# Kernel tuning notes

Hardware: AMD Instinct MI355X
Metric: run time of the kernel (lower is better)

Reference implementation:

```python
import jax, jax.numpy as jnp
import numpy as np

B, S, D, H, F = 64, 256, 512, 8, 2048
NB = 2
L = NB + 2 * NB  # blocks_1 (NB) + blocks_2 (2*NB) = 6 attention layers
DH = D // H
FC1, FC2 = 512, 256  # final_fc_dim, final_fc_dim // 2


def setup_inputs() -> dict:
    key = jax.random.key(0)
    ks = jax.random.split(key, 32)
    w = lambda k, shape, s: jax.random.normal(k, shape, dtype=jnp.float32) * s
    sD = D ** -0.5
    return {
        "q_embed_data": w(ks[0], (B, S, D), 1.0),
        "qa_embed_data": w(ks[1], (B, S, D), 1.0),
        "Wq": w(ks[2], (L, D, D), sD), "bq": jnp.zeros((L, D), jnp.float32),
        "Wk": w(ks[3], (L, D, D), sD), "bk": jnp.zeros((L, D), jnp.float32),
        "Wv": w(ks[4], (L, D, D), sD), "bv": jnp.zeros((L, D), jnp.float32),
        "Wo": w(ks[5], (L, D, D), sD), "bo": jnp.zeros((L, D), jnp.float32),
        "gammas": w(ks[6], (L, H), 1.0),
        "ln1_g": jnp.ones((L, D), jnp.float32), "ln1_b": jnp.zeros((L, D), jnp.float32),
        "W1": w(ks[7], (L, D, F), sD), "b1": jnp.zeros((L, F), jnp.float32),
        "W2": w(ks[8], (L, F, D), F ** -0.5), "b2": jnp.zeros((L, D), jnp.float32),
        "ln2_g": jnp.ones((L, D), jnp.float32), "ln2_b": jnp.zeros((L, D), jnp.float32),
        "O1": w(ks[9], (2 * D, FC1), (2 * D) ** -0.5), "bO1": jnp.zeros((FC1,), jnp.float32),
        "O2": w(ks[10], (FC1, FC2), FC1 ** -0.5), "bO2": jnp.zeros((FC2,), jnp.float32),
        "O3": w(ks[11], (FC2, 1), FC2 ** -0.5), "bO3": jnp.zeros((1,), jnp.float32),
    }


def _layer_norm(x, g, b):
    mu = x.mean(-1, keepdims=True)
    var = ((x - mu) ** 2).mean(-1, keepdims=True)
    return (x - mu) * jax.lax.rsqrt(var + 1e-5) * g + b


def _akt_attention(q, k, v, mask, gamma, zero_pad):
    # q,k,v: [B,H,S,DH]; mask: [S,S] bool; gamma: [H]
    neg = jnp.float32(-1e32)
    scores = jnp.einsum('bhqd,bhkd->bhqk', q, k) / np.sqrt(DH).astype(np.float32)
    # monotonic distance-decay (detached in the original): softmax'd scores -> cumulative distance
    sm = jax.nn.softmax(jnp.where(mask, scores, neg), axis=-1) * mask
    sm = jax.lax.stop_gradient(sm)
    distcum = jnp.cumsum(sm, axis=-1)
    disttot = jnp.sum(sm, axis=-1, keepdims=True)
    idx = jnp.arange(S)
    pos = jnp.abs(idx[:, None] - idx[None, :]).astype(jnp.float32)  # |x1 - x2|
    dist = jnp.sqrt(jnp.clip((disttot - distcum) * pos, 0.0, None))
    g = -jax.nn.softplus(gamma)[None, :, None, None]
    total_effect = jnp.clip(jnp.exp(dist * g), 1e-5, 1e5)
    scores = jnp.where(mask, scores * total_effect, neg)
    attn = jax.nn.softmax(scores, axis=-1)
    if zero_pad:
        attn = attn.at[:, :, 0, :].set(0.0)  # zero first query row
    out = jnp.einsum('bhqk,bhkd->bhqd', attn, v)
    return out, attn


def reference(q_embed_data, qa_embed_data, Wq, bq, Wk, bk, Wv, bv, Wo, bo, gammas,
              ln1_g, ln1_b, W1, b1, W2, b2, ln2_g, ln2_b, O1, bO1, O2, bO2, O3, bO3):
    idx = jnp.arange(S)
    mask_incl = idx[:, None] >= idx[None, :]  # mask==1: current + past
    mask_excl = idx[:, None] > idx[None, :]   # mask==0: strictly past

    def block(i, query, key_, vals, incl, zero_pad, apply_pos):
        proj = lambda x, W, b: (x @ W + b).reshape(B, S, H, DH).transpose(0, 2, 1, 3)
        qh, kh, vh = proj(query, Wq[i], bq[i]), proj(key_, Wk[i], bk[i]), proj(vals, Wv[i], bv[i])
        o, attn = _akt_attention(qh, kh, vh, mask_incl if incl else mask_excl, gammas[i], zero_pad)
        o = o.transpose(0, 2, 1, 3).reshape(B, S, D) @ Wo[i] + bo[i]
        q2 = _layer_norm(query + o, ln1_g[i], ln1_b[i])
        if apply_pos:
            h = jax.nn.relu(q2 @ W1[i] + b1[i]) @ W2[i] + b2[i]
            q2 = _layer_norm(q2 + h, ln2_g[i], ln2_b[i])
        return q2, attn

    y = qa_embed_data
    x = q_embed_data
    li = 0
    for _ in range(NB):  # blocks_1: knowledge encoder, self-attn, mask=1
        y, _ = block(li, y, y, y, incl=True, zero_pad=False, apply_pos=True)
        li += 1
    attn = None
    flag_first = True
    for _ in range(2 * NB):  # blocks_2: alternating question self-attn / knowledge retriever
        if flag_first:
            x, _ = block(li, x, x, x, incl=True, zero_pad=False, apply_pos=False)
            flag_first = False
        else:
            x, attn = block(li, x, x, y, incl=False, zero_pad=True, apply_pos=True)
            flag_first = True
        li += 1

    concat_q = jnp.concatenate([x, q_embed_data], axis=-1)  # [B,S,2D]
    h = jax.nn.relu(concat_q @ O1 + bO1)
    h = jax.nn.relu(h @ O2 + bO2)
    preds = jax.nn.sigmoid((h @ O3 + bO3)[..., 0])  # [B,S]
    return preds
```

## Files before the change

### kernel.cpp

```cpp
#include <hip/hip_runtime.h>

typedef unsigned short u16;
typedef unsigned int u32;
typedef short short8 __attribute__((ext_vector_type(8)));
typedef float f32x4 __attribute__((ext_vector_type(4)));

#define DEV static __device__ __forceinline__

DEV u16 f2bf(float f) {
  u32 u = __builtin_bit_cast(u32, f);
  u32 r = u + 0x7FFFu + ((u >> 16) & 1u);
  return (u16)(r >> 16);
}
DEV float bf2f(u16 h) { u32 u = ((u32)h) << 16; return __builtin_bit_cast(float, u); }

DEV u32 cvtpk(float lo, float hi_) {
  u32 r;
  asm("v_cvt_pk_bf16_f32 %0, %1, %2" : "=v"(r) : "v"(lo), "v"(hi_));
  return r;
}

DEV void async16(const u16* g, u16* l) {
  __builtin_amdgcn_global_load_lds((const __attribute__((address_space(1))) void*)g,
                                   (__attribute__((address_space(3))) void*)l, 16, 0, 0);
}

template<bool RELU, bool OUTBF, bool RESID, bool SPLIT3>
__global__ __launch_bounds__(256, 2) void gemm_kernel(
    const u16* __restrict__ A, const u16* __restrict__ A2, int KA,
    int lda, int lda2,
    const u16* __restrict__ Bt, int K,
    const float* __restrict__ bias, const float* __restrict__ resid,
    float* __restrict__ Cf, u16* __restrict__ Cb, u16* __restrict__ Cb2, u16* __restrict__ Cb3,
    int ldc)
{
  __shared__ u16 smem[2][16384];
  const int tid = threadIdx.x, wave = tid >> 6, lane = tid & 63;
  const int m0 = blockIdx.x * 128, n0 = blockIdx.y * 128;
  const int wr = wave >> 1, wc = wave & 1;
  const int lj = lane & 15, hi = lane >> 4;

  f32x4 acc[4][4];
  const f32x4 zz = {0.f, 0.f, 0.f, 0.f};
#pragma unroll
  for (int i = 0; i < 4; i++)
#pragma unroll
    for (int j = 0; j < 4; j++) acc[i][j] = zz;

  const int nkt = K / 64;

  auto stage = [&](int buf, int kt) {
    int kofs = kt * 64;
    const u16* sa; int la;
    if (kofs < KA) { sa = A + kofs; la = lda; }
    else           { sa = A2 + (kofs - KA); la = lda2; }
#pragma unroll
    for (int i = 0; i < 8; i++) {
      int c = wave * 8 + i;
      if (c < 16) {
        const u16* g = sa + (size_t)(m0 + c * 8 + (lane >> 3)) * la + (lane & 7) * 8;
        async16(g, &smem[buf][c * 512]);
      } else {
        const u16* g = Bt + (size_t)(n0 + (c - 16) * 8 + (lane >> 3)) * K + kofs + (lane & 7) * 8;
        async16(g, &smem[buf][c * 512]);
      }
    }
  };

  stage(0, 0);
  int cur = 0;
  for (int kt = 0; kt < nkt; kt++) {
    __syncthreads();
    if (kt + 1 < nkt) stage(cur ^ 1, kt + 1);
    const u16* la_ = &smem[cur][0];
    const u16* lb_ = &smem[cur][8192];
#pragma unroll
    for (int ks = 0; ks < 2; ks++) {
      short8 af[4], bfr[4];
#pragma unroll
      for (int mi = 0; mi < 4; mi++)
        af[mi] = *(const short8*)(la_ + (wr * 64 + mi * 16 + lj) * 64 + ks * 32 + hi * 8);
#pragma unroll
      for (int ni = 0; ni < 4; ni++)
        bfr[ni] = *(const short8*)(lb_ + (wc * 64 + ni * 16 + lj) * 64 + ks * 32 + hi * 8);
#pragma unroll
      for (int mi = 0; mi < 4; mi++)
#pragma unroll
        for (int ni = 0; ni < 4; ni++)
          acc[mi][ni] = __builtin_amdgcn_mfma_f32_16x16x32_bf16(af[mi], bfr[ni], acc[mi][ni], 0, 0, 0);
    }
    cur ^= 1;
  }

  u16* outB = Cb;
  int nloc = n0;
  if (SPLIT3) {
    int sec = n0 >> 9;
    outB = (sec == 0) ? Cb : (sec == 1) ? Cb2 : Cb3;
    nloc = n0 & 511;
  }

  float bv[4];
#pragma unroll
  for (int ni = 0; ni < 4; ni++) bv[ni] = bias[n0 + wc * 64 + ni * 16 + lj];
#pragma unroll
  for (int mi = 0; mi < 4; mi++)
#pragma unroll
    for (int r = 0; r < 4; r++) {
      int row = m0 + wr * 64 + mi * 16 + hi * 4 + r;
      size_t rb = (size_t)row * ldc;
#pragma unroll
      for (int ni = 0; ni < 4; ni++) {
        int col = nloc + wc * 64 + ni * 16 + lj;
        float v = acc[mi][ni][r] + bv[ni];
        if (RESID) v += resid[rb + col];
        if (RELU) v = fmaxf(v, 0.f);
        if (OUTBF) outB[rb + col] = f2bf(v);
        else Cf[rb + col] = v;
      }
    }
}

template<bool RELU, bool SPLIT3>
__global__ __launch_bounds__(512) void gemm256_kernel(
    const u16* __restrict__ A, int lda,
    const u16* __restrict__ Bt, int K,
    const float* __restrict__ bias,
    u16* __restrict__ Cb, u16* __restrict__ Cb2, u16* __restrict__ Cb3, int ldc)
{
  __shared__ u16 smem[65536];
  const int tid = threadIdx.x, wave = tid >> 6, lane = tid & 63;
  const int m0 = blockIdx.x * 256, n0 = blockIdx.y * 256;
  const int wm = wave >> 2, wn = wave & 3;
  const int lj = lane & 15, hi = lane >> 4;
  const int srow = wave * 8 + (lane >> 3);
  const int schunk = (lane & 7) ^ ((lane >> 3) & 7);

  f32x4 acc[8][4];
  const f32x4 zz = {0.f, 0.f, 0.f, 0.f};
#pragma unroll
  for (int i = 0; i < 8; i++)
#pragma unroll
    for (int j = 0; j < 4; j++) acc[i][j] = zz;

  const int nkt = K / 64;

  auto stageA = [&](int buf, int kt, int seg) {
    const u16* g = A + (size_t)(m0 + seg * 64 + srow) * lda + kt * 64 + schunk * 8;
    async16(g, &smem[buf * 16384 + (seg * 64 + wave * 8) * 64]);
  };
  auto stageB = [&](int buf, int kt, int seg) {
    const u16* g = Bt + (size_t)(n0 + seg * 64 + srow) * K + kt * 64 + schunk * 8;
    async16(g, &smem[32768 + buf * 16384 + (seg * 64 + wave * 8) * 64]);
  };

#pragma unroll
  for (int seg = 0; seg < 4; seg++) stageA(0, 0, seg);
#pragma unroll
  for (int seg = 0; seg < 4; seg++) stageB(0, 0, seg);

  int cur = 0;
  for (int t = 0; t < nkt; t++) {
    const bool pf = (t + 1 < nkt);
    const char* aB = (const char*)smem + cur * 32768;
    const char* bB = (const char*)smem + 65536 + cur * 32768;
#pragma unroll
    for (int ph = 0; ph < 4; ph++) {
      const int mh = ph >> 1, nh = ph & 1;
      if (pf) {
        if (ph < 2) { stageA(cur ^ 1, t + 1, ph * 2); stageA(cur ^ 1, t + 1, ph * 2 + 1); }
        else        { stageB(cur ^ 1, t + 1, (ph - 2) * 2); stageB(cur ^ 1, t + 1, (ph - 2) * 2 + 1); }
      }
      if (ph == 0) {
        if (pf) asm volatile("s_waitcnt vmcnt(2)" ::: "memory");
        else    asm volatile("s_waitcnt vmcnt(0)" ::: "memory");
      }
      __builtin_amdgcn_s_barrier();

      short8 af[4][2], bfr[2][2];
#pragma unroll
      for (int mi = 0; mi < 4; mi++) {
        int row = wm * 128 + (mh * 4 + mi) * 16 + lj;
#pragma unroll
        for (int ks = 0; ks < 2; ks++)
          af[mi][ks] = *(const short8*)(aB + row * 128 + ((ks * 64 + hi * 16) ^ ((row & 7) << 4)));
      }
#pragma unroll
      for (int ni = 0; ni < 2; ni++) {
        int row = wn * 64 + (nh * 2 + ni) * 16 + lj;
#pragma unroll
        for (int ks = 0; ks < 2; ks++)
          bfr[ni][ks] = *(const short8*)(bB + row * 128 + ((ks * 64 + hi * 16) ^ ((row & 7) << 4)));
      }
      __builtin_amdgcn_s_setprio(1);
#pragma unroll
      for (int mi = 0; mi < 4; mi++)
#pragma unroll
        for (int ni = 0; ni < 2; ni++)
#pragma unroll
          for (int ks = 0; ks < 2; ks++)
            acc[mh * 4 + mi][nh * 2 + ni] =
                __builtin_amdgcn_mfma_f32_16x16x32_bf16(af[mi][ks], bfr[ni][ks],
                                                        acc[mh * 4 + mi][nh * 2 + ni], 0, 0, 0);
      __builtin_amdgcn_s_setprio(0);
      __builtin_amdgcn_s_barrier();
    }
    cur ^= 1;
  }

  u16* outB = Cb;
  int nloc = n0;
  if (SPLIT3) {
    int sec = n0 >> 9;
    outB = (sec == 0) ? Cb : (sec == 1) ? Cb2 : Cb3;
    nloc = n0 & 511;
  }

  float bv[4];
#pragma unroll
  for (int ni = 0; ni < 4; ni++) bv[ni] = bias[n0 + wn * 64 + ni * 16 + lj];
#pragma unroll
  for (int mi = 0; mi < 8; mi++)
#pragma unroll
    for (int r = 0; r < 4; r++) {
      int row = m0 + wm * 128 + mi * 16 + hi * 4 + r;
      size_t rb = (size_t)row * ldc;
#pragma unroll
      for (int ni = 0; ni < 4; ni++) {
        int col = nloc + wn * 64 + ni * 16 + lj;
        float v = acc[mi][ni][r] + bv[ni];
        if (RELU) v = fmaxf(v, 0.f);
        outB[rb + col] = f2bf(v);
      }
    }
}

template<bool INCL, bool ZP>
__global__ __launch_bounds__(512) void attn_kernel(
    const u16* __restrict__ qb, const u16* __restrict__ kb, const u16* __restrict__ vb,
    u16* __restrict__ ob, const float* __restrict__ gammas, int li)
{
  __shared__ u16 smem[32768];
  const int tid = threadIdx.x, wave = tid >> 6, lane = tid & 63;
  const int h = blockIdx.x, b = blockIdx.y;
  const int lj = lane & 15, hi = lane >> 4;
  const size_t rowbase = (size_t)b * 256 * 512 + h * 64;

#pragma unroll
  for (int p = 0; p < 2; p++) {
    int r2 = p * 128 + (tid >> 3) * 2;
    int cc = (tid & 7) * 8;
    union { uint4 v; u16 e[8]; } v0, v1;
    uint4 k0 = *(const uint4*)(kb + rowbase + (size_t)r2 * 512 + cc);
    uint4 k1 = *(const uint4*)(kb + rowbase + (size_t)(r2 + 1) * 512 + cc);
    v0.v = *(const uint4*)(vb + rowbase + (size_t)r2 * 512 + cc);
    v1.v = *(const uint4*)(vb + rowbase + (size_t)(r2 + 1) * 512 + cc);
    *(uint4*)((char*)smem + r2 * 128 + ((cc * 2) ^ ((r2 & 7) << 4))) = k0;
    *(uint4*)((char*)smem + (r2 + 1) * 128 + ((cc * 2) ^ (((r2 + 1) & 7) << 4))) = k1;
#pragma unroll
    for (int i = 0; i < 8; i++) {
      int d = cc + i;
      u32 pk = (u32)v0.e[i] | ((u32)v1.e[i] << 16);
      *(u32*)((char*)smem + 32768 + d * 512 + ((2 * r2) ^ ((d & 7) << 4))) = pk;
    }
  }

  const int qt0 = wave, qt1 = 15 - wave;

  short8 qfa[2][2];
#pragma unroll
  for (int cf = 0; cf < 2; cf++) {
    int t = cf ? qt1 : qt0;
#pragma unroll
    for (int s = 0; s < 2; s++)
      qfa[cf][s] = *(const short8*)(qb + rowbase + (size_t)(t * 16 + lj) * 512 + s * 32 + hi * 8);
  }

  float gm = gammas[li * 8 + h];
  float geff = -(gm > 20.f ? gm : log1pf(__expf(gm)));

  __syncthreads();

  const f32x4 zz = {0.f, 0.f, 0.f, 0.f};
  const int hsel = hi >> 1;
  const int sbase = lj + 32 * (hi & 1);

#pragma unroll
  for (int cf = 0; cf < 2; cf++) {
    const int t = cf ? qt1 : qt0;
    const int qb0 = t * 16;
    const int q = qb0 + lj;
    const int nrf = t + 1;
    const int nsp = (t + 2) >> 1;

    f32x4 acc[16], E[16];
#pragma unroll
    for (int rf = 0; rf < 16; rf++) acc[rf] = zz;

#pragma unroll
    for (int rf = 0; rf < 16; rf++) {
      if (rf >= nrf) continue;
      int row = rf * 16 + lj;
#pragma unroll
      for (int s = 0; s < 2; s++) {
        short8 kf = *(const short8*)((char*)smem + row * 128 + ((s * 64 + hi * 16) ^ ((row & 7) << 4)));
        acc[rf] = __builtin_amdgcn_mfma_f32_16x16x32_bf16(kf, qfa[cf][s], acc[rf], 0, 0, 0);
      }
    }

    float mx = -1e30f;
#pragma unroll
    for (int rf = 0; rf < 16; rf++) {
      if (rf >= nrf) continue;
#pragma unroll
      for (int r = 0; r < 4; r++) {
        acc[rf][r] *= 0.125f;
        int k = rf * 16 + hi * 4 + r;
        bool valid = INCL ? (k <= q) : (k < q);
        mx = fmaxf(mx, valid ? acc[rf][r] : -1e30f);
      }
    }
    mx = fmaxf(mx, __shfl_xor(mx, 16));
    mx = fmaxf(mx, __shfl_xor(mx, 32));
    float sum = 0.f;
#pragma unroll
    for (int rf = 0; rf < 16; rf++) {
      if (rf >= nrf) continue;
#pragma unroll
      for (int r = 0; r < 4; r++) {
        int k = rf * 16 + hi * 4 + r;
        bool valid = INCL ? (k <= q) : (k < q);
        float ev = valid ? __expf(acc[rf][r] - mx) : 0.f;
        E[rf][r] = ev;
        sum += ev;
      }
    }
    sum += __shfl_xor(sum, 16);
    sum += __shfl_xor(sum, 32);
    float inv1 = sum > 0.f ? 1.f / sum : 0.f;
    float dtot = sum > 0.f ? 1.f : 0.f;

    float run = 0.f;
#pragma unroll
    for (int rf = 0; rf < 16; rf++) {
      if (rf >= nrf) continue;
      float p[4];
      float pa = 0.f;
#pragma unroll
      for (int r = 0; r < 4; r++) {
        pa += E[rf][r] * inv1;
        p[r] = pa;
      }
      float tl = p[3];
      float v = tl;
      float u1 = __shfl_up(v, 16); v += (hi >= 1) ? u1 : 0.f;
      float u2 = __shfl_up(v, 32); v += (hi >= 2) ? u2 : 0.f;
      float T = __shfl(v, lj + 48);
      float cbase = run + (v - tl);
#pragma unroll
      for (int r = 0; r < 4; r++) {
        int k = rf * 16 + hi * 4 + r;
        bool valid = INCL ? (k <= q) : (k < q);
        float tail = fmaxf(dtot - (cbase + p[r]), 0.f);
        float pos = (float)(q - k);
        float dist = sqrtf(tail * pos);
        float te = fmaxf(__expf(dist * geff), 1e-5f);
        acc[rf][r] = valid ? acc[rf][r] * te : -1e32f;
      }
      run += T;
    }

    float mx2 = -3.0e38f;
#pragma unroll
    for (int rf = 0; rf < 16; rf++) {
      if (rf >= nrf) continue;
#pragma unroll
      for (int r = 0; r < 4; r++) mx2 = fmaxf(mx2, acc[rf][r]);
    }
    mx2 = fmaxf(mx2, __shfl_xor(mx2, 16));
    mx2 = fmaxf(mx2, __shfl_xor(mx2, 32));
    float sum2 = 0.f;
#pragma unroll
    for (int rf = 0; rf < 16; rf++) {
      if (rf >= nrf) continue;
#pragma unroll
      for (int r = 0; r < 4; r++) {
        float ev = __expf(acc[rf][r] - mx2);
        acc[rf][r] = ev;
        sum2 += ev;
      }
    }
    sum2 += __shfl_xor(sum2, 16);
    sum2 += __shfl_xor(sum2, 32);
    float inv = 1.f / sum2;
    if (ZP) { if (q == 0) inv = 0.f; }
#pragma unroll
    for (int rf = 0; rf < 16; rf++) {
      if (rf >= nrf) continue;
#pragma unroll
      for (int r = 0; r < 4; r++) acc[rf][r] *= inv;
    }

    f32x4 oacc[4];
#pragma unroll
    for (int j = 0; j < 4; j++) oacc[j] = zz;

#pragma unroll
    for (int sp = 0; sp < 8; sp++) {
      if (sp >= nsp) continue;
      u32 a0 = cvtpk(acc[2 * sp][0],     acc[2 * sp][1]);
      u32 a1 = cvtpk(acc[2 * sp][2],     acc[2 * sp][3]);
      u32 b0 = cvtpk(acc[2 * sp + 1][0], acc[2 * sp + 1][1]);
      u32 b1 = cvtpk(acc[2 * sp + 1][2], acc[2 * sp + 1][3]);
      u32 pw[4];
#pragma unroll
      for (int tt = 0; tt < 4; tt++) {
        int src = sbase + 16 * (tt >> 1);
        u32 za = (u32)__shfl((int)((tt & 1) ? a1 : a0), src);
        u32 zb = (u32)__shfl((int)((tt & 1) ? b1 : b0), src);
        pw[tt] = hsel ? zb : za;
      }
      short8 pf = __builtin_bit_cast(short8, *(uint4*)pw);
#pragma unroll
      for (int nf = 0; nf < 4; nf++) {
        int d = nf * 16 + lj;
        short8 vf = *(const short8*)((char*)smem + 32768 + d * 512 + ((sp * 64 + hi * 16) ^ ((d & 7) << 4)));
        oacc[nf] = __builtin_amdgcn_mfma_f32_16x16x32_bf16(pf, vf, oacc[nf], 0, 0, 0);
      }
    }

#pragma unroll
    for (int r = 0; r < 4; r++) {
      int qr = qb0 + hi * 4 + r;
      size_t obase = (size_t)(b * 256 + qr) * 512 + h * 64;
#pragma unroll
      for (int nf = 0; nf < 4; nf++)
        ob[obase + nf * 16 + lj] = f2bf(oacc[nf][r]);
    }
  }
}

__global__ __launch_bounds__(256) void ln_kernel(const float* __restrict__ x,
    const float* __restrict__ g, const float* __restrict__ bt,
    float* __restrict__ outF, u16* __restrict__ outB)
{
  int row = blockIdx.x * 4 + (threadIdx.x >> 6), lane = threadIdx.x & 63;
  const float* xr = x + (size_t)row * 512 + lane * 8;
  float4 a = *(const float4*)xr;
  float4 c = *(const float4*)(xr + 4);
  float s = a.x + a.y + a.z + a.w + c.x + c.y + c.z + c.w;
  float q = a.x*a.x + a.y*a.y + a.z*a.z + a.w*a.w + c.x*c.x + c.y*c.y + c.z*c.z + c.w*c.w;
#pragma unroll
  for (int m = 1; m <= 32; m <<= 1) { s += __shfl_xor(s, m); q += __shfl_xor(q, m); }
  float mu = s * (1.f / 512.f);
  float var = q * (1.f / 512.f) - mu * mu;
  float rs = rsqrtf(fmaxf(var, 0.f) + 1e-5f);
  const float* gr = g + lane * 8; const float* br = bt + lane * 8;
  float4 g0 = *(const float4*)gr, g1v = *(const float4*)(gr + 4);
  float4 b0 = *(const float4*)br, b1v = *(const float4*)(br + 4);
  float y[8];
  y[0]=(a.x-mu)*rs*g0.x+b0.x; y[1]=(a.y-mu)*rs*g0.y+b0.y; y[2]=(a.z-mu)*rs*g0.z+b0.z; y[3]=(a.w-mu)*rs*g0.w+b0.w;
  y[4]=(c.x-mu)*rs*g1v.x+b1v.x; y[5]=(c.y-mu)*rs*g1v.y+b1v.y; y[6]=(c.z-mu)*rs*g1v.z+b1v.z; y[7]=(c.w-mu)*rs*g1v.w+b1v.w;
  float* of = outF + (size_t)row * 512 + lane * 8;
  *(float4*)of = make_float4(y[0], y[1], y[2], y[3]);
  *(float4*)(of + 4) = make_float4(y[4], y[5], y[6], y[7]);
  union { uint4 v; u16 e[8]; } pk;
#pragma unroll
  for (int i = 0; i < 8; i++) pk.e[i] = f2bf(y[i]);
  *(uint4*)(outB + (size_t)row * 512 + lane * 8) = pk.v;
}

__global__ void cvt_kernel(const float* __restrict__ in, u16* __restrict__ out, int n8)
{
  int i = blockIdx.x * 256 + threadIdx.x;
  if (i >= n8) return;
  float4 a = ((const float4*)in)[2 * i], c = ((const float4*)in)[2 * i + 1];
  union { uint4 v; u16 e[8]; } pk;
  pk.e[0]=f2bf(a.x); pk.e[1]=f2bf(a.y); pk.e[2]=f2bf(a.z); pk.e[3]=f2bf(a.w);
  pk.e[4]=f2bf(c.x); pk.e[5]=f2bf(c.y); pk.e[6]=f2bf(c.z); pk.e[7]=f2bf(c.w);
  ((uint4*)out)[i] = pk.v;
}

__global__ void trans_kernel(const float* __restrict__ in, u16* __restrict__ out,
                             int R, int C, size_t istr, size_t ostr)
{
  __shared__ float tile[32][33];
  in += (size_t)blockIdx.z * istr;
  out += (size_t)blockIdx.z * ostr;
  int c0 = blockIdx.x * 32, r0 = blockIdx.y * 32;
  int tx = threadIdx.x & 31, ty = threadIdx.x >> 5;
#pragma unroll
  for (int i = 0; i < 4; i++) tile[ty + i * 8][tx] = in[(size_t)(r0 + ty + i * 8) * C + c0 + tx];
  __syncthreads();
#pragma unroll
  for (int i = 0; i < 4; i++) out[(size_t)(c0 + ty + i * 8) * R + r0 + tx] = f2bf(tile[tx][ty + i * 8]);
}

__global__ void bias_concat_kernel(const float* __restrict__ bq, const float* __restrict__ bk,
                                   const float* __restrict__ bv, float* __restrict__ out)
{
  int t = blockIdx.x * 256 + threadIdx.x;
  if (t >= 6 * 1536) return;
  int li = t / 1536, c = t % 1536;
  float v = (c < 512) ? bq[li * 512 + c]
          : (c < 1024) ? bk[li * 512 + c - 512]
                       : bv[li * 512 + c - 1024];
  out[t] = v;
}

__global__ __launch_bounds__(256) void pred_kernel(const u16* __restrict__ h2,
    const float* __restrict__ O3, const float* __restrict__ bO3, float* __restrict__ out)
{
  int row = blockIdx.x * 4 + (threadIdx.x >> 6), lane = threadIdx.x & 63;
  union { uint2 v; u16 e[4]; } hv;
  hv.v = *(const uint2*)(h2 + (size_t)row * 256 + lane * 4);
  float d = 0.f;
#pragma unroll
  for (int i = 0; i < 4; i++) d += bf2f(hv.e[i]) * O3[lane * 4 + i];
#pragma unroll
  for (int m = 1; m <= 32; m <<= 1) d += __shfl_xor(d, m);
  if (lane == 0) out[row] = 1.f / (1.f + expf(-(d + bO3[0])));
}

extern "C" void kernel_launch(void* const* d_in, const int* in_sizes, int n_in,
                              void* d_out, int out_size, void* d_ws, size_t ws_size,
                              hipStream_t stream)
{
  const float* qe   = (const float*)d_in[0];
  const float* qa   = (const float*)d_in[1];
  const float* Wq   = (const float*)d_in[2];  const float* bq  = (const float*)d_in[3];
  const float* Wk   = (const float*)d_in[4];  const float* bk  = (const float*)d_in[5];
  const float* Wv   = (const float*)d_in[6];  const float* bv  = (const float*)d_in[7];
  const float* Wo   = (const float*)d_in[8];  const float* bo  = (const float*)d_in[9];
  const float* gam  = (const float*)d_in[10];
  const float* ln1g = (const float*)d_in[11]; const float* ln1b = (const float*)d_in[12];
  const float* W1   = (const float*)d_in[13]; const float* b1  = (const float*)d_in[14];
  const float* W2   = (const float*)d_in[15]; const float* b2  = (const float*)d_in[16];
  const float* ln2g = (const float*)d_in[17]; const float* ln2b = (const float*)d_in[18];
  const float* O1   = (const float*)d_in[19]; const float* bO1 = (const float*)d_in[20];
  const float* O2   = (const float*)d_in[21]; const float* bO2 = (const float*)d_in[22];
  const float* O3   = (const float*)d_in[23]; const float* bO3 = (const float*)d_in[24];
  float* preds = (float*)d_out;

  const int M = 16384;
  const int BIG = 0x3fffffff;
  char* ws = (char*)d_ws;
  size_t off = 0;
  auto alloc = [&](size_t bytes) { char* p = ws + off; off += (bytes + 255) & ~(size_t)255; return p; };

  u16* wqkvt = (u16*)alloc((size_t)6*1536*512*2);
  u16* wot   = (u16*)alloc((size_t)6*512*512*2);
  u16* w1t   = (u16*)alloc((size_t)6*2048*512*2);
  u16* w2t   = (u16*)alloc((size_t)6*512*2048*2);
  u16* o1t   = (u16*)alloc((size_t)512*1024*2);
  u16* o2t   = (u16*)alloc((size_t)256*512*2);
  float* bqkv = (float*)alloc((size_t)6*1536*4);
  u16* qx  = (u16*)alloc((size_t)M*512*2);
  u16* sA  = (u16*)alloc((size_t)M*512*2);
  u16* sB  = (u16*)alloc((size_t)M*512*2);
  float* g1 = (float*)alloc((size_t)M*512*4);
  u16* region = (u16*)alloc((size_t)M*2048*2);
  u16* qbf = region;
  u16* kbf = region + (size_t)M*512;
  u16* vbf = region + (size_t)2*M*512;
  u16* obf = region + (size_t)3*M*512;
  u16* h1  = region;
  u16* hd1 = region;
  u16* hd2 = region + (size_t)2*M*512;
  (void)ws_size; (void)in_sizes; (void)n_in; (void)out_size;

  trans_kernel<<<dim3(16, 16, 6), 256, 0, stream>>>(Wq, wqkvt,                          512, 512,  (size_t)512*512,  (size_t)1536*512);
  trans_kernel<<<dim3(16, 16, 6), 256, 0, stream>>>(Wk, wqkvt + (size_t)512*512,        512, 512,  (size_t)512*512,  (size_t)1536*512);
  trans_kernel<<<dim3(16, 16, 6), 256, 0, stream>>>(Wv, wqkvt + (size_t)1024*512,       512, 512,  (size_t)512*512,  (size_t)1536*512);
  trans_kernel<<<dim3(16, 16, 6), 256, 0, stream>>>(Wo, wot,                            512, 512,  (size_t)512*512,  (size_t)512*512);
  trans_kernel<<<dim3(64, 16, 6), 256, 0, stream>>>(W1, w1t,                            512, 2048, (size_t)512*2048, (size_t)2048*512);
  trans_kernel<<<dim3(16, 64, 6), 256, 0, stream>>>(W2, w2t,                            2048, 512, (size_t)2048*512, (size_t)512*2048);
  trans_kernel<<<dim3(16, 32, 1), 256, 0, stream>>>(O1, o1t,                            1024, 512, 0, 0);
  trans_kernel<<<dim3(8, 16, 1),  256, 0, stream>>>(O2, o2t,                            512, 256,  0, 0);
  bias_concat_kernel<<<36, 256, 0, stream>>>(bq, bk, bv, bqkv);
  cvt_kernel<<<4096, 256, 0, stream>>>(qe, qx, M * 512 / 8);
  cvt_kernel<<<4096, 256, 0, stream>>>(qa, sA, M * 512 / 8);

  const u16* curB = sA;
  const float* curF = qa;
  const u16* yfin = nullptr;
  const dim3 gP(128, 4), gA(8, 64);

  for (int li = 0; li < 6; li++) {
    bool ffn  = (li == 0 || li == 1 || li == 3 || li == 5);
    bool excl = (li == 3 || li == 5);
    size_t wqkv_off = (size_t)li * 1536 * 512;

    if (!excl) {
      gemm256_kernel<false, true><<<dim3(64, 6), 512, 0, stream>>>(
          curB, 512, wqkvt + wqkv_off, 512, bqkv + li * 1536, qbf, kbf, vbf, 512);
    } else {
      gemm256_kernel<false, true><<<dim3(64, 4), 512, 0, stream>>>(
          curB, 512, wqkvt + wqkv_off, 512, bqkv + li * 1536, qbf, kbf, nullptr, 512);
      gemm_kernel<false, true, false, false><<<dim3(128, 4), 256, 0, stream>>>(
          yfin, yfin, BIG, 512, 512, wqkvt + wqkv_off + (size_t)1024 * 512, 512, bv + li * 512,
          nullptr, nullptr, vbf, nullptr, nullptr, 512);
    }

    if (!excl) attn_kernel<true,  false><<<gA, 512, 0, stream>>>(qbf, kbf, vbf, obf, gam, li);
    else       attn_kernel<false, true ><<<gA, 512, 0, stream>>>(qbf, kbf, vbf, obf, gam, li);

    gemm_kernel<false, false, true, false><<<gP, 256, 0, stream>>>(
        obf, obf, BIG, 512, 512, wot + (size_t)li * 512 * 512, 512, bo + li * 512,
        curF, g1, nullptr, nullptr, nullptr, 512);

    ln_kernel<<<4096, 256, 0, stream>>>(g1, ln1g + li * 512, ln1b + li * 512, g1, sB);
    curB = sB; curF = g1;

    if (ffn) {
      gemm256_kernel<true, false><<<dim3(64, 8), 512, 0, stream>>>(
          curB, 512, w1t + (size_t)li * 2048 * 512, 512, b1 + li * 2048, h1, nullptr, nullptr, 2048);
      gemm_kernel<false, false, true, false><<<gP, 256, 0, stream>>>(
          h1, h1, BIG, 2048, 2048, w2t + (size_t)li * 512 * 2048, 2048, b2 + li * 512,
          g1, g1, nullptr, nullptr, nullptr, 512);
      u16* nB = (li < 2) ? sA : sB;
      ln_kernel<<<4096, 256, 0, stream>>>(g1, ln2g + li * 512, ln2b + li * 512, g1, nB);
      curB = nB;
    }
    if (li == 1) { yfin = curB; curB = qx; curF = qe; }
  }

  gemm_kernel<true, true, false, false><<<dim3(128, 4), 256, 0, stream>>>(
      curB, qx, 512, 512, 512, o1t, 1024, bO1, nullptr, nullptr, hd1, nullptr, nullptr, 512);
  gemm_kernel<true, true, false, false><<<dim3(128, 2), 256, 0, stream>>>(
      hd1, hd1, BIG, 512, 512, o2t, 512, bO2, nullptr, nullptr, hd2, nullptr, nullptr, 256);
  pred_kernel<<<4096, 256, 0, stream>>>(hd2, O3, bO3, preds);
}
```

Before: 1.331 ms.

## Fuse output-projection and FFN2 GEMMs with residual add and LayerNorm

Adds a GEMM kernel whose block owns 64 full rows of the 512-wide output, with a double-buffered async LDS pipeline. Its epilogue adds bias and residual, reduces row mean and variance across waves through shared memory, and writes normalized fp32 and bf16 outputs. This replaces the separate Wo/W2 GEMMs and the standalone LayerNorm kernels, removing a full fp32 write and read of the activation plus extra launches. In exchange each block needs about 147KB of LDS, so only one block fits per CU, and the grid shrinks to 256 blocks, which may leave the GEMM latency-bound.

```diff
diff --git a/kernel.cpp b/kernel.cpp
--- a/kernel.cpp
+++ b/kernel.cpp
@@ -231,6 +231,143 @@
         float v = acc[mi][ni][r] + bv[ni];
         if (RELU) v = fmaxf(v, 0.f);
         outB[rb + col] = f2bf(v);
+      }
+    }
+}
+
+__global__ __launch_bounds__(512) void gemmln_kernel(
+    const u16* __restrict__ A, int lda,
+    const u16* __restrict__ Bt, int K,
+    const float* __restrict__ bias, const float* __restrict__ resid,
+    const float* __restrict__ gamma, const float* __restrict__ beta,
+    float* __restrict__ outF, u16* __restrict__ outB)
+{
+  __shared__ u16 smem[73728];
+  const int tid = threadIdx.x, wave = tid >> 6, lane = tid & 63;
+  const int m0 = blockIdx.x * 64;
+  const int lj = lane & 15, hi = lane >> 4;
+  const int srow = lane >> 3;
+  const int schunk = (lane & 7) ^ ((lane >> 3) & 7);
+
+  f32x4 acc[4][4];
+  const f32x4 zz = {0.f, 0.f, 0.f, 0.f};
+#pragma unroll
+  for (int i = 0; i < 4; i++)
+#pragma unroll
+    for (int j = 0; j < 4; j++) acc[i][j] = zz;
+
+  const int nkt = K / 64;
+
+  auto stageA = [&](int buf, int kt) {
+    const u16* g = A + (size_t)(m0 + wave * 8 + srow) * lda + kt * 64 + schunk * 8;
+    async16(g, &smem[buf * 4096 + (wave * 8) * 64]);
+  };
+  auto stageB = [&](int buf, int kt, int seg) {
+    const u16* g = Bt + (size_t)(seg * 64 + wave * 8 + srow) * K + kt * 64 + schunk * 8;
+    async16(g, &smem[8192 + buf * 32768 + (seg * 64 + wave * 8) * 64]);
+  };
+
+  stageA(0, 0);
+#pragma unroll
+  for (int seg = 0; seg < 8; seg++) stageB(0, 0, seg);
+
+  int cur = 0;
+  for (int t = 0; t < nkt; t++) {
+    const bool pf = (t + 1 < nkt);
+    const char* aB = (const char*)smem + cur * 8192;
+    const char* bB = (const char*)smem + 16384 + cur * 65536;
+#pragma unroll
+    for (int ph = 0; ph < 4; ph++) {
+      const int mh = ph >> 1, nh = ph & 1;
+      if (pf) {
+        if (ph == 0) { stageA(cur ^ 1, t + 1); stageB(cur ^ 1, t + 1, 0); stageB(cur ^ 1, t + 1, 1); }
+        else { stageB(cur ^ 1, t + 1, ph * 2); stageB(cur ^ 1, t + 1, ph * 2 + 1); }
+      }
+      if (ph == 0) {
+        if (pf) asm volatile("s_waitcnt vmcnt(3)" ::: "memory");
+        else    asm volatile("s_waitcnt vmcnt(0)" ::: "memory");
+      }
+      __builtin_amdgcn_s_barrier();
+
+      short8 af[2][2], bfr[2][2];
+#pragma unroll
+      for (int mi = 0; mi < 2; mi++) {
+        int row = (mh * 2 + mi) * 16 + lj;
+#pragma unroll
+        for (int ks = 0; ks < 2; ks++)
+          af[mi][ks] = *(const short8*)(aB + row * 128 + ((ks * 64 + hi * 16) ^ ((row & 7) << 4)));
+      }
+#pragma unroll
+      for (int ni = 0; ni < 2; ni++) {
+        int row = wave * 64 + (nh * 2 + ni) * 16 + lj;
+#pragma unroll
+        for (int ks = 0; ks < 2; ks++)
+          bfr[ni][ks] = *(const short8*)(bB + row * 128 + ((ks * 64 + hi * 16) ^ ((row & 7) << 4)));
+      }
+      __builtin_amdgcn_s_setprio(1);
+#pragma unroll
+      for (int mi = 0; mi < 2; mi++)
+#pragma unroll
+        for (int ni = 0; ni < 2; ni++)
+#pragma unroll
+          for (int ks = 0; ks < 2; ks++)
+            acc[mh * 2 + mi][nh * 2 + ni] =
+                __builtin_amdgcn_mfma_f32_16x16x32_bf16(af[mi][ks], bfr[ni][ks],
+                                                        acc[mh * 2 + mi][nh * 2 + ni], 0, 0, 0);
+      __builtin_amdgcn_s_setprio(0);
+      __builtin_amdgcn_s_barrier();
+    }
+    cur ^= 1;
+  }
+
+  float bv[4], gv[4], btv[4];
+  int col[4];
+#pragma unroll
+  for (int ni = 0; ni < 4; ni++) {
+    col[ni] = wave * 64 + ni * 16 + lj;
+    bv[ni] = bias[col[ni]];
+    gv[ni] = gamma[col[ni]];
+    btv[ni] = beta[col[ni]];
+  }
+
+  float* red = (float*)smem;
+
+#pragma unroll
+  for (int mi = 0; mi < 4; mi++)
+#pragma unroll
+    for (int r = 0; r < 4; r++) {
+      int lrow = mi * 16 + hi * 4 + r;
+      size_t rb = (size_t)(m0 + lrow) * 512;
+      float s = 0.f, q = 0.f;
+#pragma unroll
+      for (int ni = 0; ni < 4; ni++) {
+        float v = acc[mi][ni][r] + bv[ni] + resid[rb + col[ni]];
+        acc[mi][ni][r] = v;
+        s += v; q += v * v;
+      }
+#pragma unroll
+      for (int m = 1; m <= 8; m <<= 1) { s += __shfl_xor(s, m); q += __shfl_xor(q, m); }
+      if (lj == 0) { red[lrow * 16 + wave * 2] = s; red[lrow * 16 + wave * 2 + 1] = q; }
+    }
+  __syncthreads();
+
+#pragma unroll
+  for (int mi = 0; mi < 4; mi++)
+#pragma unroll
+    for (int r = 0; r < 4; r++) {
+      int lrow = mi * 16 + hi * 4 + r;
+      size_t rb = (size_t)(m0 + lrow) * 512;
+      float s = 0.f, q = 0.f;
+#pragma unroll
+      for (int w = 0; w < 8; w++) { s += red[lrow * 16 + w * 2]; q += red[lrow * 16 + w * 2 + 1]; }
+      float mu = s * (1.f / 512.f);
+      float var = q * (1.f / 512.f) - mu * mu;
+      float rs = rsqrtf(fmaxf(var, 0.f) + 1e-5f);
+#pragma unroll
+      for (int ni = 0; ni < 4; ni++) {
+        float y = (acc[mi][ni][r] - mu) * rs * gv[ni] + btv[ni];
+        outF[rb + col[ni]] = y;
+        outB[rb + col[ni]] = f2bf(y);
       }
     }
 }
@@ -438,36 +575,6 @@
         ob[obase + nf * 16 + lj] = f2bf(oacc[nf][r]);
     }
   }
-}
-
-__global__ __launch_bounds__(256) void ln_kernel(const float* __restrict__ x,
-    const float* __restrict__ g, const float* __restrict__ bt,
-    float* __restrict__ outF, u16* __restrict__ outB)
-{
-  int row = blockIdx.x * 4 + (threadIdx.x >> 6), lane = threadIdx.x & 63;
-  const float* xr = x + (size_t)row * 512 + lane * 8;
-  float4 a = *(const float4*)xr;
-  float4 c = *(const float4*)(xr + 4);
-  float s = a.x + a.y + a.z + a.w + c.x + c.y + c.z + c.w;
-  float q = a.x*a.x + a.y*a.y + a.z*a.z + a.w*a.w + c.x*c.x + c.y*c.y + c.z*c.z + c.w*c.w;
-#pragma unroll
-  for (int m = 1; m <= 32; m <<= 1) { s += __shfl_xor(s, m); q += __shfl_xor(q, m); }
-  float mu = s * (1.f / 512.f);
-  float var = q * (1.f / 512.f) - mu * mu;
-  float rs = rsqrtf(fmaxf(var, 0.f) + 1e-5f);
-  const float* gr = g + lane * 8; const float* br = bt + lane * 8;
-  float4 g0 = *(const float4*)gr, g1v = *(const float4*)(gr + 4);
-  float4 b0 = *(const float4*)br, b1v = *(const float4*)(br + 4);
-  float y[8];
-  y[0]=(a.x-mu)*rs*g0.x+b0.x; y[1]=(a.y-mu)*rs*g0.y+b0.y; y[2]=(a.z-mu)*rs*g0.z+b0.z; y[3]=(a.w-mu)*rs*g0.w+b0.w;
-  y[4]=(c.x-mu)*rs*g1v.x+b1v.x; y[5]=(c.y-mu)*rs*g1v.y+b1v.y; y[6]=(c.z-mu)*rs*g1v.z+b1v.z; y[7]=(c.w-mu)*rs*g1v.w+b1v.w;
-  float* of = outF + (size_t)row * 512 + lane * 8;
-  *(float4*)of = make_float4(y[0], y[1], y[2], y[3]);
-  *(float4*)(of + 4) = make_float4(y[4], y[5], y[6], y[7]);
-  union { uint4 v; u16 e[8]; } pk;
-#pragma unroll
-  for (int i = 0; i < 8; i++) pk.e[i] = f2bf(y[i]);
-  *(uint4*)(outB + (size_t)row * 512 + lane * 8) = pk.v;
 }
 
 __global__ void cvt_kernel(const float* __restrict__ in, u16* __restrict__ out, int n8)
@@ -584,7 +691,7 @@
   const u16* curB = sA;
   const float* curF = qa;
   const u16* yfin = nullptr;
-  const dim3 gP(128, 4), gA(8, 64);
+  const dim3 gA(8, 64);
 
   for (int li = 0; li < 6; li++) {
     bool ffn  = (li == 0 || li == 1 || li == 3 || li == 5);
@@ -605,21 +712,18 @@
     if (!excl) attn_kernel<true,  false><<<gA, 512, 0, stream>>>(qbf, kbf, vbf, obf, gam, li);
     else       attn_kernel<false, true ><<<gA, 512, 0, stream>>>(qbf, kbf, vbf, obf, gam, li);
 
-    gemm_kernel<false, false, true, false><<<gP, 256, 0, stream>>>(
-        obf, obf, BIG, 512, 512, wot + (size_t)li * 512 * 512, 512, bo + li * 512,
-        curF, g1, nullptr, nullptr, nullptr, 512);
-
-    ln_kernel<<<4096, 256, 0, stream>>>(g1, ln1g + li * 512, ln1b + li * 512, g1, sB);
+    gemmln_kernel<<<256, 512, 0, stream>>>(
+        obf, 512, wot + (size_t)li * 512 * 512, 512, bo + li * 512,
+        curF, ln1g + li * 512, ln1b + li * 512, g1, sB);
     curB = sB; curF = g1;
 
     if (ffn) {
       gemm256_kernel<true, false><<<dim3(64, 8), 512, 0, stream>>>(
           curB, 512, w1t + (size_t)li * 2048 * 512, 512, b1 + li * 2048, h1, nullptr, nullptr, 2048);
-      gemm_kernel<false, false, true, false><<<gP, 256, 0, stream>>>(
-          h1, h1, BIG, 2048, 2048, w2t + (size_t)li * 512 * 2048, 2048, b2 + li * 512,
-          g1, g1, nullptr, nullptr, nullptr, 512);
       u16* nB = (li < 2) ? sA : sB;
-      ln_kernel<<<4096, 256, 0, stream>>>(g1, ln2g + li * 512, ln2b + li * 512, g1, nB);
+      gemmln_kernel<<<256, 512, 0, stream>>>(
+          h1, 2048, w2t + (size_t)li * 512 * 2048, 2048, b2 + li * 512,
+          g1, ln2g + li * 512, ln2b + li * 512, g1, nB);
       curB = nB;
     }
     if (li == 1) { yfin = curB; curB = qx; curF = qe; }
```

Result: faster. 1.269 ms (-4.7%).
